# Kernel tuning notes

Measured on AMD Instinct MI355X. Metric: run time of the kernel, lower is better.

The kernel has to match this reference:

```python
import jax, jax.numpy as jnp
import numpy as np
from jax import lax

INPUT, HIDDEN, OUTPUT = 128, 1024, 128
BATCH, T_STEPS = 256, 512


def _uniform(key, shape, fan_in):
    bound = 1.0 / np.sqrt(fan_in)
    return jax.random.uniform(key, shape, jnp.float32, -bound, bound)


def setup_inputs() -> dict:
    key = jax.random.key(0)
    ks = jax.random.split(key, 7)
    return {
        "x_0": jax.random.normal(ks[0], (BATCH, INPUT), jnp.float32),
        "W_i2h": _uniform(ks[1], (INPUT, HIDDEN), INPUT),
        "b_i2h": _uniform(ks[2], (HIDDEN,), INPUT),
        "W_h2h": _uniform(ks[3], (HIDDEN, HIDDEN), HIDDEN),
        "b_h2h": _uniform(ks[4], (HIDDEN,), HIDDEN),
        "W_h2o": _uniform(ks[5], (HIDDEN, OUTPUT), HIDDEN),
        "b_h2o": _uniform(ks[6], (OUTPUT,), HIDDEN),
        "T": T_STEPS,
    }


def reference(x_0, W_i2h, b_i2h, W_h2h, b_h2h, W_h2o, b_h2o, T):
    batch = x_0.shape[0]
    h0 = jnp.zeros((batch, W_h2h.shape[0]), x_0.dtype)

    def step(carry, _):
        x, h = carry
        # hidden_pre = i2h(x) + h2h(h); hidden = tanh(hidden_pre)
        h = jnp.tanh(x @ W_i2h + b_i2h + h @ W_h2h + b_h2h)
        x_out = h @ W_h2o + b_h2o  # fed back as next input
        return (x_out, h), x_out

    _, ys = lax.scan(step, (x_0, h0), None, length=T - 1)
    # trajectory[0] = x_0, trajectory[t+1] = x_output at step t
    return jnp.concatenate([x_0[None], ys], axis=0)  # [T, B, output]
```

## Files before the change

### kernel.cpp

```cpp
#include <hip/hip_runtime.h>
#include <cstdint>
#include <cstddef>


#define BATCH  256
#define INPUT  128
#define HIDDEN 1024
#define OUTPUT 128
#define TSTEPS 512
#define NCAT   1152
#define NTILE  72
#define GROUPS 16
#define MEMB   16
#define NSLOT  4

#define WS_WFRAG 0u
#define WS_BEFF  2621440u
#define WS_HBUF  2629632u
#define WS_BAR   4726784u
#define BAR_U32S 768

typedef _Float16 f16;
typedef _Float16 v8h __attribute__((ext_vector_type(8)));
typedef float    v4f __attribute__((ext_vector_type(4)));

__device__ __forceinline__ float fast_tanh(float x){
  float e = __expf(2.0f * x);
  return (e - 1.0f) / (e + 1.0f);
}

__global__ void k_bias(const float* __restrict__ bi2h, const float* __restrict__ bh2h,
                       const float* __restrict__ bh2o, const float* __restrict__ Wi2h,
                       float* __restrict__ beff){
  int n = blockIdx.x*256 + threadIdx.x;
  if (n >= 1168) return;
  float v = 0.f;
  if (n < HIDDEN){
    v = bi2h[n] + bh2h[n];
    for (int j=0;j<INPUT;j++) v += bh2o[j]*Wi2h[j*HIDDEN + n];
  } else if (n < NCAT){
    v = bh2o[n - HIDDEN];
  }
  beff[n] = v;
}

__global__ void k_h1(const float* __restrict__ x0, const float* __restrict__ Wi2h,
                     const float* __restrict__ bi2h, const float* __restrict__ bh2h,
                     f16* __restrict__ hbuf){
  int idx = blockIdx.x*256 + threadIdx.x;
  int m = idx >> 10, n = idx & 1023;
  float acc = bi2h[n] + bh2h[n];
  const float* xr = x0 + m*INPUT;
  for (int j=0;j<INPUT;j++) acc += xr[j]*Wi2h[j*HIDDEN + n];
  hbuf[idx] = (f16)fast_tanh(acc);
}

__global__ void k_copy0(const float* __restrict__ x0, float* __restrict__ out){
  int i = blockIdx.x*256 + threadIdx.x;
  out[i] = x0[i];
}

__global__ void k_wfrag(const float* __restrict__ Wh2h, const float* __restrict__ Wh2o,
                        const float* __restrict__ Wi2h, f16* __restrict__ Wfrag){
  int gid = blockIdx.x*256 + threadIdx.x;
  int lane = gid & 63;
  int fi = gid >> 6;
  int c = fi % 5, kk = (fi/5) & 7, wv = (fi/40) & 3, mem = fi/160;
  int k0 = wv*256 + kk*32 + (lane>>4)*8;
  int n  = mem*NTILE + c*16 + (lane & 15);
  f16 vals[8];
  if (n >= NCAT){
    #pragma unroll
    for (int j=0;j<8;j++) vals[j] = (f16)0.f;
  } else if (n >= HIDDEN){
    #pragma unroll
    for (int j=0;j<8;j++) vals[j] = (f16)Wh2o[(k0+j)*OUTPUT + (n-HIDDEN)];
  } else {
    float acc[8];
    #pragma unroll
    for (int j=0;j<8;j++) acc[j] = Wh2h[(k0+j)*HIDDEN + n];
    for (int q=0;q<INPUT;q++){
      float wi = Wi2h[q*HIDDEN + n];
      #pragma unroll
      for (int j=0;j<8;j++) acc[j] += Wh2o[(k0+j)*OUTPUT + q]*wi;
    }
    #pragma unroll
    for (int j=0;j<8;j++) vals[j] = (f16)acc[j];
  }
  v8h pack;
  #pragma unroll
  for (int j=0;j<8;j++) pack[j] = vals[j];
  *(v8h*)(Wfrag + (size_t)gid*8) = pack;
}

__global__ void __launch_bounds__(256, 1)
k_rnn(const f16* __restrict__ Wfrag, const float* __restrict__ beff,
      f16* __restrict__ hbuf, unsigned int* __restrict__ bar,
      float* __restrict__ out){
  extern __shared__ char lds_raw[];
  float*    red    = (float*)lds_raw;
  unsigned* s_slot = (unsigned*)(lds_raw + 16384);

  const int tid  = threadIdx.x;
  const int lane = tid & 63;
  const int wv   = tid >> 6;

  if (tid == 0){
    unsigned xcc;
    asm volatile("s_getreg_b32 %0, hwreg(HW_REG_XCC_ID)" : "=s"(xcc));
    xcc &= 7;
    unsigned slot = atomicAdd(&bar[512 + xcc*32], 1u);
    *s_slot = xcc*32 + (slot & 31u);
  }
  __syncthreads();
  const unsigned sid = *s_slot;
  const int g   = sid >> 4;
  const int mem = sid & 15;
  if (g >= GROUPS) return;
  const int m0   = g * 16;
  const int n0   = mem * NTILE;
  const int quad = lane >> 4;
  const int l15  = lane & 15;

  v8h bw[8][5];
  {
    const f16* wp = Wfrag + ((size_t)((mem*4 + wv)*40)*64 + lane)*8;
    #pragma unroll
    for (int kk=0;kk<8;kk++)
      #pragma unroll
      for (int c=0;c<5;c++)
        bw[kk][c] = *(const v8h*)(wp + (size_t)((kk*5+c)*64)*8);
  }

  const int kbase = wv*256;
  unsigned int* cnt = bar + g*32;

  for (int t=1; t<TSTEPS; ++t){
    const f16* hin  = hbuf + (size_t)((t-1)&(NSLOT-1))*(BATCH*HIDDEN);
    f16*       hout = hbuf + (size_t)(t&(NSLOT-1))*(BATCH*HIDDEN);

    v8h af[8];
    {
      const v8h* abase = (const v8h*)(hin + (size_t)(m0 + l15)*HIDDEN + kbase + quad*8);
      #pragma unroll
      for (int kk=0;kk<8;kk++)
        af[kk] = abase[kk*4];
    }

    v4f acc[5];
    #pragma unroll
    for (int c=0;c<5;c++){ v4f z = {0.f,0.f,0.f,0.f}; acc[c] = z; }

    #pragma unroll
    for (int kk=0;kk<8;kk++){
      #pragma unroll
      for (int c=0;c<5;c++)
        acc[c] = __builtin_amdgcn_mfma_f32_16x16x32_f16(af[kk], bw[kk][c], acc[c], 0,0,0);
    }

    #pragma unroll
    for (int c=0;c<5;c++){
      int owner = c & 3;
      if (wv != owner){
        int rank = (wv > owner) ? wv-1 : wv;
        *(v4f*)(red + ((size_t)(c*3 + rank)*64 + lane)*4) = acc[c];
      }
    }
    __syncthreads();

    #pragma unroll
    for (int c=0;c<5;c++){
      if ((c & 3) == wv){
        int colT = c*16 + l15;
        int col  = n0 + colT;
        if (col < HIDDEN && colT < NTILE){
          v4f s = acc[c];
          #pragma unroll
          for (int r=0;r<3;r++) s += *(const v4f*)(red + ((size_t)(c*3 + r)*64 + lane)*4);
          float b = beff[col];
          #pragma unroll
          for (int r=0;r<4;r++){
            float v = fast_tanh(s[r] + b);
            hout[(size_t)(m0 + quad*4 + r)*HIDDEN + col] = (f16)v;
          }
        }
      }
    }
    __syncthreads();
    if (tid == 0){
      atomicAdd(cnt, 1u);
    }
    #pragma unroll
    for (int c=0;c<5;c++){
      if ((c & 3) == wv){
        int colT = c*16 + l15;
        int col  = n0 + colT;
        if (col >= HIDDEN && colT < NTILE){
          v4f s = acc[c];
          #pragma unroll
          for (int r=0;r<3;r++) s += *(const v4f*)(red + ((size_t)(c*3 + r)*64 + lane)*4);
          float b = beff[col];
          float* op = out + (size_t)t*(BATCH*OUTPUT) + (col - HIDDEN);
          #pragma unroll
          for (int r=0;r<4;r++)
            op[(size_t)(m0 + quad*4 + r)*OUTPUT] = s[r] + b;
        }
      }
    }
    if (tid == 0){
      unsigned tries = 0;
      while (__hip_atomic_load(cnt, __ATOMIC_RELAXED, __HIP_MEMORY_SCOPE_AGENT)
             < (unsigned)(MEMB*t) && tries < 2048u){
        __builtin_amdgcn_s_sleep(1);
        ++tries;
      }
    }
    __syncthreads();
  }
}

extern "C" void kernel_launch(void* const* d_in, const int* in_sizes, int n_in,
                              void* d_out, int out_size, void* d_ws, size_t ws_size,
                              hipStream_t stream){
  const float* x0   = (const float*)d_in[0];
  const float* Wi2h = (const float*)d_in[1];
  const float* bi2h = (const float*)d_in[2];
  const float* Wh2h = (const float*)d_in[3];
  const float* bh2h = (const float*)d_in[4];
  const float* Wh2o = (const float*)d_in[5];
  const float* bh2o = (const float*)d_in[6];
  float* out = (float*)d_out;
  char* ws = (char*)d_ws;

  f16*          Wfrag = (f16*)(ws + WS_WFRAG);
  float*        beff  = (float*)(ws + WS_BEFF);
  f16*          hbuf  = (f16*)(ws + WS_HBUF);
  unsigned int* bar   = (unsigned int*)(ws + WS_BAR);

  hipMemsetAsync(bar, 0, BAR_U32S*sizeof(unsigned int), stream);
  k_bias <<<5,    256, 0, stream>>>(bi2h, bh2h, bh2o, Wi2h, beff);
  k_h1   <<<1024, 256, 0, stream>>>(x0, Wi2h, bi2h, bh2h, hbuf);
  k_copy0<<<128,  256, 0, stream>>>(x0, out);
  k_wfrag<<<640,  256, 0, stream>>>(Wh2h, Wh2o, Wi2h, Wfrag);

  hipFuncSetAttribute((const void*)k_rnn, hipFuncAttributeMaxDynamicSharedMemorySize, 98304);
  k_rnn<<<256, 256, 98304, stream>>>(Wfrag, beff, hbuf, bar, out);
}
```

Before: 1.679 ms.

## Replace group counter barrier with per-wave flag polling and double-buffered LDS

The per-block atomic counter barrier with thread-0 spinning and two __syncthreads is replaced by per-wave flags: each wave stores its step number after its stores drain, and every wave polls all 64 flags of its group with a wave-wide __all before reading h. The LDS reduction buffer is double-buffered by step parity so the trailing block barrier can be dropped, and biases are hoisted into registers. This cuts barrier latency and lets waves proceed independently. It risks memory-ordering issues because it relies on relaxed atomics plus vmcnt waits with no release fence, and the spin loop has a bounded timeout.

Result: slower. 3.667 ms (+118.4%).

```diff
diff --git a/kernel.cpp b/kernel.cpp
--- a/kernel.cpp
+++ b/kernel.cpp
@@ -18,7 +18,7 @@
 #define WS_BEFF  2621440u
 #define WS_HBUF  2629632u
 #define WS_BAR   4726784u
-#define BAR_U32S 768
+#define BAR_U32S 1280
 
 typedef _Float16 f16;
 typedef _Float16 v8h __attribute__((ext_vector_type(8)));
@@ -98,8 +98,7 @@
       f16* __restrict__ hbuf, unsigned int* __restrict__ bar,
       float* __restrict__ out){
   extern __shared__ char lds_raw[];
-  float*    red    = (float*)lds_raw;
-  unsigned* s_slot = (unsigned*)(lds_raw + 16384);
+  unsigned* s_slot = (unsigned*)(lds_raw + 32768);
 
   const int tid  = threadIdx.x;
   const int lane = tid & 63;
@@ -109,7 +108,7 @@
     unsigned xcc;
     asm volatile("s_getreg_b32 %0, hwreg(HW_REG_XCC_ID)" : "=s"(xcc));
     xcc &= 7;
-    unsigned slot = atomicAdd(&bar[512 + xcc*32], 1u);
+    unsigned slot = atomicAdd(&bar[1024 + xcc*32], 1u);
     *s_slot = xcc*32 + (slot & 31u);
   }
   __syncthreads();
@@ -132,12 +131,35 @@
         bw[kk][c] = *(const v8h*)(wp + (size_t)((kk*5+c)*64)*8);
   }
 
+  float bown[2] = {0.f, 0.f};
+  #pragma unroll
+  for (int c=0;c<5;c++){
+    if ((c & 3) == wv){
+      int colT = c*16 + l15;
+      int col  = n0 + colT;
+      if (colT < NTILE && col < NCAT) bown[c>>2] = beff[col];
+    }
+  }
+
   const int kbase = wv*256;
-  unsigned int* cnt = bar + g*32;
+  unsigned int* flg  = bar + g*64;
+  const int   myflag = mem*4 + wv;
 
   for (int t=1; t<TSTEPS; ++t){
+    {
+      const unsigned target = (unsigned)(t-1);
+      unsigned tries = 0;
+      for (;;){
+        unsigned f = __hip_atomic_load(flg + lane, __ATOMIC_RELAXED,
+                                       __HIP_MEMORY_SCOPE_AGENT);
+        if (__all((int)(f >= target))) break;
+        if (++tries > 4096u) break;
+      }
+    }
+
     const f16* hin  = hbuf + (size_t)((t-1)&(NSLOT-1))*(BATCH*HIDDEN);
     f16*       hout = hbuf + (size_t)(t&(NSLOT-1))*(BATCH*HIDDEN);
+    float*     red  = (float*)(lds_raw + (size_t)(t & 1)*16384);
 
     v8h af[8];
     {
@@ -177,7 +199,7 @@
           v4f s = acc[c];
           #pragma unroll
           for (int r=0;r<3;r++) s += *(const v4f*)(red + ((size_t)(c*3 + r)*64 + lane)*4);
-          float b = beff[col];
+          float b = bown[c>>2];
           #pragma unroll
           for (int r=0;r<4;r++){
             float v = fast_tanh(s[r] + b);
@@ -186,10 +208,12 @@
         }
       }
     }
-    __syncthreads();
-    if (tid == 0){
-      atomicAdd(cnt, 1u);
-    }
+
+    asm volatile("s_waitcnt vmcnt(0)" ::: "memory");
+    if (lane == 0)
+      __hip_atomic_store(flg + myflag, (unsigned)t, __ATOMIC_RELAXED,
+                         __HIP_MEMORY_SCOPE_AGENT);
+
     #pragma unroll
     for (int c=0;c<5;c++){
       if ((c & 3) == wv){
@@ -199,7 +223,7 @@
           v4f s = acc[c];
           #pragma unroll
           for (int r=0;r<3;r++) s += *(const v4f*)(red + ((size_t)(c*3 + r)*64 + lane)*4);
-          float b = beff[col];
+          float b = bown[c>>2];
           float* op = out + (size_t)t*(BATCH*OUTPUT) + (col - HIDDEN);
           #pragma unroll
           for (int r=0;r<4;r++)
@@ -207,15 +231,6 @@
         }
       }
     }
-    if (tid == 0){
-      unsigned tries = 0;
-      while (__hip_atomic_load(cnt, __ATOMIC_RELAXED, __HIP_MEMORY_SCOPE_AGENT)
-             < (unsigned)(MEMB*t) && tries < 2048u){
-        __builtin_amdgcn_s_sleep(1);
-        ++tries;
-      }
-    }
-    __syncthreads();
   }
 }
 
```

## Interleave two batch groups per block with per-member flag sync

Applied to the files above, without the earlier changes.

Each block now handles two batch groups (A and B) on the same XCC, alternating their recurrence steps so that waiting on one group's barrier overlaps with computing the other's. The shared atomic counter is replaced by per-member step flags, which a wave polls across 16 lanes. Bias values are also hoisted into registers. Only 16 blocks per XCC do work now (128 total), which halves parallelism and doubles serial work per block. It relies on the XCC-to-group mapping, and the bounded spin timeouts could let stale data through.

Measured after the change: 2.252 ms. 34.1% more time.

```diff
diff --git a/kernel.cpp b/kernel.cpp
--- a/kernel.cpp
+++ b/kernel.cpp
@@ -93,13 +93,99 @@
   *(v8h*)(Wfrag + (size_t)gid*8) = pack;
 }
 
+#define CHAIN_STEP(M0X, REDX, FLGX)                                              \
+  do {                                                                           \
+    if (wv == 0){                                                                \
+      const unsigned target = (unsigned)(t-1);                                   \
+      unsigned tries = 0;                                                        \
+      for (;;){                                                                  \
+        unsigned f = __hip_atomic_load((FLGX) + (lane & 15), __ATOMIC_RELAXED,   \
+                                       __HIP_MEMORY_SCOPE_AGENT);                \
+        if (__all((int)(f >= target))) break;                                    \
+        if (++tries > 2048u) break;                                              \
+        __builtin_amdgcn_s_sleep(1);                                             \
+      }                                                                          \
+    }                                                                            \
+    __syncthreads();             \
+    const f16* hin  = hbuf + (size_t)((t-1)&(NSLOT-1))*(BATCH*HIDDEN);           \
+    f16*       hout = hbuf + (size_t)(t&(NSLOT-1))*(BATCH*HIDDEN);               \
+    v8h af[8];                                                                   \
+    {                                                                            \
+      const v8h* abase = (const v8h*)(hin + (size_t)((M0X) + l15)*HIDDEN         \
+                                      + kbase + quad*8);                         \
+      _Pragma("unroll")                                                          \
+      for (int kk=0;kk<8;kk++) af[kk] = abase[kk*4];                             \
+    }                                                                            \
+    v4f acc[5];                                                                  \
+    _Pragma("unroll")                                                            \
+    for (int c=0;c<5;c++){ v4f z = {0.f,0.f,0.f,0.f}; acc[c] = z; }              \
+    _Pragma("unroll")                                                            \
+    for (int kk=0;kk<8;kk++){                                                    \
+      _Pragma("unroll")                                                          \
+      for (int c=0;c<5;c++)                                                      \
+        acc[c] = __builtin_amdgcn_mfma_f32_16x16x32_f16(af[kk], bw[kk][c],       \
+                                                        acc[c], 0,0,0);          \
+    }                                                                            \
+    _Pragma("unroll")                                                            \
+    for (int c=0;c<5;c++){                                                       \
+      int owner = c & 3;                                                         \
+      if (wv != owner){                                                          \
+        int rank = (wv > owner) ? wv-1 : wv;                                     \
+        *(v4f*)((REDX) + ((size_t)(c*3 + rank)*64 + lane)*4) = acc[c];           \
+      }                                                                          \
+    }                                                                            \
+    __syncthreads();                                      \
+    _Pragma("unroll")                                                            \
+    for (int c=0;c<5;c++){                                                       \
+      if ((c & 3) == wv){                                                        \
+        int colT = c*16 + l15;                                                   \
+        int col  = n0 + colT;                                                    \
+        if (col < HIDDEN && colT < NTILE){                                       \
+          v4f s = acc[c];                                                        \
+          _Pragma("unroll")                                                      \
+          for (int r=0;r<3;r++)                                                  \
+            s += *(const v4f*)((REDX) + ((size_t)(c*3 + r)*64 + lane)*4);        \
+          float b = bown[c>>2];                                                  \
+          _Pragma("unroll")                                                      \
+          for (int r=0;r<4;r++){                                                 \
+            float v = fast_tanh(s[r] + b);                                       \
+            hout[(size_t)((M0X) + quad*4 + r)*HIDDEN + col] = (f16)v;            \
+          }                                                                      \
+        }                                                                        \
+      }                                                                          \
+    }                                                                            \
+    __syncthreads();         \
+    if (tid == 0)                                                                \
+      __hip_atomic_store((FLGX) + mem, (unsigned)t, __ATOMIC_RELAXED,            \
+                         __HIP_MEMORY_SCOPE_AGENT);                              \
+    _Pragma("unroll")                                                            \
+    for (int c=0;c<5;c++){                                                       \
+      if ((c & 3) == wv){                                                        \
+        int colT = c*16 + l15;                                                   \
+        int col  = n0 + colT;                                                    \
+        if (col >= HIDDEN && colT < NTILE){                                      \
+          v4f s = acc[c];                                                        \
+          _Pragma("unroll")                                                      \
+          for (int r=0;r<3;r++)                                                  \
+            s += *(const v4f*)((REDX) + ((size_t)(c*3 + r)*64 + lane)*4);        \
+          float b = bown[c>>2];                                                  \
+          float* op = out + (size_t)t*(BATCH*OUTPUT) + (col - HIDDEN);           \
+          _Pragma("unroll")                                                      \
+          for (int r=0;r<4;r++)                                                  \
+            op[(size_t)((M0X) + quad*4 + r)*OUTPUT] = s[r] + b;                  \
+        }                                                                        \
+      }                                                                          \
+    }                                                                            \
+  } while(0)
+
 __global__ void __launch_bounds__(256, 1)
 k_rnn(const f16* __restrict__ Wfrag, const float* __restrict__ beff,
       f16* __restrict__ hbuf, unsigned int* __restrict__ bar,
       float* __restrict__ out){
   extern __shared__ char lds_raw[];
-  float*    red    = (float*)lds_raw;
-  unsigned* s_slot = (unsigned*)(lds_raw + 16384);
+  float*    redA   = (float*)lds_raw;
+  float*    redB   = (float*)(lds_raw + 16384);
+  unsigned* s_slot = (unsigned*)(lds_raw + 32768);
 
   const int tid  = threadIdx.x;
   const int lane = tid & 63;
@@ -114,10 +200,14 @@
   }
   __syncthreads();
   const unsigned sid = *s_slot;
-  const int g   = sid >> 4;
-  const int mem = sid & 15;
-  if (g >= GROUPS) return;
-  const int m0   = g * 16;
+  const int xcc  = sid >> 5;
+  const int slot = sid & 31;
+  if (slot >= MEMB) return;
+  const int mem = slot;
+  const int gA  = xcc;
+  const int gB  = xcc + 8;
+  const int m0A = gA * 16;
+  const int m0B = gB * 16;
   const int n0   = mem * NTILE;
   const int quad = lane >> 4;
   const int l15  = lane & 15;
@@ -132,90 +222,23 @@
         bw[kk][c] = *(const v8h*)(wp + (size_t)((kk*5+c)*64)*8);
   }
 
+  float bown[2] = {0.f, 0.f};
+  #pragma unroll
+  for (int c=0;c<5;c++){
+    if ((c & 3) == wv){
+      int colT = c*16 + l15;
+      int col  = n0 + colT;
+      if (colT < NTILE && col < NCAT) bown[c>>2] = beff[col];
+    }
+  }
+
   const int kbase = wv*256;
-  unsigned int* cnt = bar + g*32;
+  unsigned int* flgA = bar + gA*32;
+  unsigned int* flgB = bar + gB*32;
 
   for (int t=1; t<TSTEPS; ++t){
-    const f16* hin  = hbuf + (size_t)((t-1)&(NSLOT-1))*(BATCH*HIDDEN);
-    f16*       hout = hbuf + (size_t)(t&(NSLOT-1))*(BATCH*HIDDEN);
-
-    v8h af[8];
-    {
-      const v8h* abase = (const v8h*)(hin + (size_t)(m0 + l15)*HIDDEN + kbase + quad*8);
-      #pragma unroll
-      for (int kk=0;kk<8;kk++)
-        af[kk] = abase[kk*4];
-    }
-
-    v4f acc[5];
-    #pragma unroll
-    for (int c=0;c<5;c++){ v4f z = {0.f,0.f,0.f,0.f}; acc[c] = z; }
-
-    #pragma unroll
-    for (int kk=0;kk<8;kk++){
-      #pragma unroll
-      for (int c=0;c<5;c++)
-        acc[c] = __builtin_amdgcn_mfma_f32_16x16x32_f16(af[kk], bw[kk][c], acc[c], 0,0,0);
-    }
-
-    #pragma unroll
-    for (int c=0;c<5;c++){
-      int owner = c & 3;
-      if (wv != owner){
-        int rank = (wv > owner) ? wv-1 : wv;
-        *(v4f*)(red + ((size_t)(c*3 + rank)*64 + lane)*4) = acc[c];
-      }
-    }
-    __syncthreads();
-
-    #pragma unroll
-    for (int c=0;c<5;c++){
-      if ((c & 3) == wv){
-        int colT = c*16 + l15;
-        int col  = n0 + colT;
-        if (col < HIDDEN && colT < NTILE){
-          v4f s = acc[c];
-          #pragma unroll
-          for (int r=0;r<3;r++) s += *(const v4f*)(red + ((size_t)(c*3 + r)*64 + lane)*4);
-          float b = beff[col];
-          #pragma unroll
-          for (int r=0;r<4;r++){
-            float v = fast_tanh(s[r] + b);
-            hout[(size_t)(m0 + quad*4 + r)*HIDDEN + col] = (f16)v;
-          }
-        }
-      }
-    }
-    __syncthreads();
-    if (tid == 0){
-      atomicAdd(cnt, 1u);
-    }
-    #pragma unroll
-    for (int c=0;c<5;c++){
-      if ((c & 3) == wv){
-        int colT = c*16 + l15;
-        int col  = n0 + colT;
-        if (col >= HIDDEN && colT < NTILE){
-          v4f s = acc[c];
-          #pragma unroll
-          for (int r=0;r<3;r++) s += *(const v4f*)(red + ((size_t)(c*3 + r)*64 + lane)*4);
-          float b = beff[col];
-          float* op = out + (size_t)t*(BATCH*OUTPUT) + (col - HIDDEN);
-          #pragma unroll
-          for (int r=0;r<4;r++)
-            op[(size_t)(m0 + quad*4 + r)*OUTPUT] = s[r] + b;
-        }
-      }
-    }
-    if (tid == 0){
-      unsigned tries = 0;
-      while (__hip_atomic_load(cnt, __ATOMIC_RELAXED, __HIP_MEMORY_SCOPE_AGENT)
-             < (unsigned)(MEMB*t) && tries < 2048u){
-        __builtin_amdgcn_s_sleep(1);
-        ++tries;
-      }
-    }
-    __syncthreads();
+    CHAIN_STEP(m0A, redA, flgA);
+    CHAIN_STEP(m0B, redB, flgB);
   }
 }
 
```
